# Performance work log

Measured on AMD Instinct MI355X. Metric: run time of the kernel, lower is better.

The kernel has to match this reference:

```python
import jax, jax.numpy as jnp
import numpy as np

N_NODES = 80000
N_EDGES = 1280000
IN_CH = 128
HID = 64
N_GRAPHS = 64
DROPOUT_P = 0.3


def setup_inputs() -> dict:
    key = jax.random.key(0)
    ks = jax.random.split(key, 12)
    x = jax.random.normal(ks[0], (N_NODES, IN_CH), dtype=jnp.float32)
    edge_index = jax.random.randint(ks[1], (2, N_EDGES), 0, N_NODES, dtype=jnp.int64 if jax.config.read('jax_enable_x64') else jnp.int32)
    batch = jnp.sort(jax.random.randint(ks[2], (N_NODES,), 0, N_GRAPHS))
    def lin(k, fan_in, fan_out):
        lim = 1.0 / np.sqrt(fan_in)
        kw, kb = jax.random.split(k)
        W = jax.random.uniform(kw, (fan_in, fan_out), minval=-lim, maxval=lim, dtype=jnp.float32)
        b = jax.random.uniform(kb, (fan_out,), minval=-lim, maxval=lim, dtype=jnp.float32)
        return W, b
    W1, b1 = lin(ks[3], IN_CH, HID)
    W2, b2 = lin(ks[4], HID, HID)
    W3, b3 = lin(ks[5], HID, HID)
    Wm1, bm1 = lin(ks[6], HID, HID)
    Wm2, bm2 = lin(ks[7], HID, 1)
    return {"x": x, "edge_index": edge_index, "batch": batch,
            "W1": W1, "b1": b1, "W2": W2, "b2": b2, "W3": W3, "b3": b3,
            "Wm1": Wm1, "bm1": bm1, "Wm2": Wm2, "bm2": bm2}


def _gcn_conv(x, W, b, src, dst, deg_inv_sqrt):
    # PyG GCNConv: h = X W; add self-loops; norm_e = d^-1/2[src] * d^-1/2[dst]
    h = x @ W  # [N, F]
    norm = deg_inv_sqrt[src] * deg_inv_sqrt[dst]  # [E]
    agg = jax.ops.segment_sum(h[src] * norm[:, None], dst, num_segments=x.shape[0])
    agg = agg + h * (deg_inv_sqrt * deg_inv_sqrt)[:, None]  # self-loop term d^-1
    return agg + b


def _dropout(x, key, p):
    keep = jax.random.bernoulli(key, 1.0 - p, x.shape)
    return jnp.where(keep, x / (1.0 - p), 0.0)


def reference(x, edge_index, batch, W1, b1, W2, b2, W3, b3, Wm1, bm1, Wm2, bm2):
    src, dst = edge_index[0], edge_index[1]
    N = x.shape[0]
    # in-degree on dst, +1 for self-loop (PyG default normalization)
    deg = jax.ops.segment_sum(jnp.ones_like(dst, dtype=x.dtype), dst, num_segments=N) + 1.0
    deg_inv_sqrt = jax.lax.rsqrt(deg)

    dk = jax.random.split(jax.random.key(42), 4)
    h = _dropout(jax.nn.relu(_gcn_conv(x, W1, b1, src, dst, deg_inv_sqrt)), dk[0], DROPOUT_P)
    h = _dropout(jax.nn.relu(_gcn_conv(h, W2, b2, src, dst, deg_inv_sqrt)), dk[1], DROPOUT_P)
    h = _dropout(jax.nn.relu(_gcn_conv(h, W3, b3, src, dst, deg_inv_sqrt)), dk[2], DROPOUT_P)

    # global mean pool per graph
    sums = jax.ops.segment_sum(h, batch, num_segments=N_GRAPHS)
    counts = jax.ops.segment_sum(jnp.ones((N,), dtype=h.dtype), batch, num_segments=N_GRAPHS)
    pooled = sums / jnp.maximum(counts, 1.0)[:, None]  # [G, HID]

    # MLP head: Linear -> ReLU -> Dropout -> Linear
    m = jax.nn.relu(pooled @ Wm1 + bm1)
    m = _dropout(m, dk[3], DROPOUT_P)
    return m @ Wm2 + bm2  # [G, 1]
```

## Files before the change

### kernel.cpp

```cpp
#include <hip/hip_runtime.h>
#include <hip/hip_fp8.h>
#include <stdint.h>

#define HID 64
#define INCH 128
#define NGRAPH 64
#define KEEPP 0.7f
#define SCAN_B 256

typedef __attribute__((ext_vector_type(8))) short short8;
typedef __attribute__((ext_vector_type(4))) float floatx4;
typedef unsigned short ushort_t;

__device__ __forceinline__ uint8_t f2e4(float f) {
  __hip_fp8_e4m3 t(f);
  return (uint8_t)t.__x;
}
__device__ __forceinline__ float e42f(uint8_t b) {
  __hip_fp8_e4m3 t;
  t.__x = (__hip_fp8_storage_t)b;
  return (float)t;
}

__host__ __device__ inline void tf2x32(uint32_t k0, uint32_t k1,
                                       uint32_t& x0, uint32_t& x1) {
  const uint32_t ks2 = k0 ^ k1 ^ 0x1BD11BDAu;
#define ROTL32(v, d) (((v) << (d)) | ((v) >> (32 - (d))))
#define TF_RND(r) { x0 += x1; x1 = ROTL32(x1, r); x1 ^= x0; }
  x0 += k0; x1 += k1;
  TF_RND(13) TF_RND(15) TF_RND(26) TF_RND(6)
  x0 += k1;  x1 += ks2 + 1u;
  TF_RND(17) TF_RND(29) TF_RND(16) TF_RND(24)
  x0 += ks2; x1 += k0 + 2u;
  TF_RND(13) TF_RND(15) TF_RND(26) TF_RND(6)
  x0 += k0;  x1 += k1 + 3u;
  TF_RND(17) TF_RND(29) TF_RND(16) TF_RND(24)
  x0 += k1;  x1 += ks2 + 4u;
  TF_RND(13) TF_RND(15) TF_RND(26) TF_RND(6)
  x0 += ks2; x1 += k0 + 5u;
#undef TF_RND
#undef ROTL32
}

__device__ __forceinline__ bool keep_mask(uint32_t k0, uint32_t k1, uint32_t idx) {
  uint32_t x0 = 0u, x1 = idx;
  tf2x32(k0, k1, x0, x1);
  uint32_t bits = x0 ^ x1;
  float u = __uint_as_float((bits >> 9) | 0x3f800000u) - 1.0f;
  return u < KEEPP;
}

__global__ void k_hist(const int* __restrict__ dst, int E, int* __restrict__ counts) {
  int e = blockIdx.x * blockDim.x + threadIdx.x;
  if (e < E) atomicAdd(&counts[dst[e]], 1);
}

__global__ __launch_bounds__(SCAN_B) void k_scan1d(const int* __restrict__ counts,
                                                   int* __restrict__ bsum,
                                                   float* __restrict__ dinv, int N) {
  int i = blockIdx.x * SCAN_B + threadIdx.x;
  int v = 0;
  if (i < N) {
    v = counts[i];
    dinv[i] = rsqrtf((float)v + 1.0f);
  }
  int r = v;
  for (int off = 32; off > 0; off >>= 1) r += __shfl_down(r, off);
  __shared__ int ws[4];
  if ((threadIdx.x & 63) == 0) ws[threadIdx.x >> 6] = r;
  __syncthreads();
  if (threadIdx.x == 0) bsum[blockIdx.x] = ws[0] + ws[1] + ws[2] + ws[3];
}

__device__ __forceinline__ void wsplit_one(const float* __restrict__ W,
                                           short8* __restrict__ Wh,
                                           short8* __restrict__ Wl, int i) {
  int lane = i & 63, f = i >> 6;
  int kc = f >> 2, ct = f & 3;
  int kbase = kc * 32 + ((lane >> 4) << 3);
  int n = ct * 16 + (lane & 15);
  short8 h, l;
#pragma unroll
  for (int j = 0; j < 8; ++j) {
    float w = W[(size_t)(kbase + j) * HID + n];
    uint32_t u = __float_as_uint(w);
    h[j] = (short)(u >> 16);
    float r = w - __uint_as_float(u & 0xFFFF0000u);
    l[j] = (short)(__float_as_uint(r) >> 16);
  }
  Wh[i] = h;
  Wl[i] = l;
}

__global__ __launch_bounds__(1024) void k_scan2w(const int* __restrict__ bsum,
                                                 int* __restrict__ bpre, int B,
                                                 const float* __restrict__ W1,
                                                 short8* __restrict__ Wh1, short8* __restrict__ Wl1,
                                                 const float* __restrict__ W2,
                                                 short8* __restrict__ Wh2, short8* __restrict__ Wl2,
                                                 const float* __restrict__ W3,
                                                 short8* __restrict__ Wh3, short8* __restrict__ Wl3) {
  if (blockIdx.x == 0) {
    __shared__ int s[1024];
    int tid = threadIdx.x;
    int v = (tid < B) ? bsum[tid] : 0;
    s[tid] = v;
    __syncthreads();
    for (int off = 1; off < 1024; off <<= 1) {
      int t = (tid >= off) ? s[tid - off] : 0;
      __syncthreads();
      s[tid] += t;
      __syncthreads();
    }
    if (tid < B) bpre[tid] = s[tid] - v;
    return;
  }
  int b = blockIdx.x - 1;
  int tid = threadIdx.x;
  if (b == 0) {
    wsplit_one(W1, Wh1, Wl1, tid);
  } else if (b == 1 && tid < 512) {
    wsplit_one(W2, Wh2, Wl2, tid);
  } else if (b == 2 && tid < 512) {
    wsplit_one(W3, Wh3, Wl3, tid);
  }
}

__global__ __launch_bounds__(SCAN_B) void k_scan3(const int* __restrict__ counts,
                                                  const int* __restrict__ bpre,
                                                  int* __restrict__ row_off,
                                                  int* __restrict__ cursor,
                                                  int N, int E) {
  __shared__ int s[SCAN_B];
  int tid = threadIdx.x;
  int i = blockIdx.x * SCAN_B + tid;
  int v = (i < N) ? counts[i] : 0;
  s[tid] = v;
  __syncthreads();
  for (int off = 1; off < SCAN_B; off <<= 1) {
    int t = (tid >= off) ? s[tid - off] : 0;
    __syncthreads();
    s[tid] += t;
    __syncthreads();
  }
  if (i < N) {
    int excl = bpre[blockIdx.x] + s[tid] - v;
    row_off[i] = excl;
    cursor[i] = excl;
  }
  if (i == 0) row_off[N] = E;
}

template <int K>
__device__ __forceinline__ void mgemm_tile(const float* __restrict__ A,
                                           const short8* __restrict__ Wh,
                                           const short8* __restrict__ Wl,
                                           uint8_t* __restrict__ C, int N,
                                           int tile) {
  constexpr int KC = K / 32;
  const int lane = threadIdx.x & 63;
  const int wv = threadIdx.x >> 6;
  const int m = lane & 15;
  const int q = lane >> 4;
  const int row0 = tile * 64 + wv * 16;
  if (row0 >= N) return;
  const int arow = min(row0 + m, N - 1);
  const float* __restrict__ ap = A + (size_t)arow * K + (q << 3);

  floatx4 acc[4];
#pragma unroll
  for (int ct = 0; ct < 4; ++ct) acc[ct] = (floatx4){0.f, 0.f, 0.f, 0.f};

#pragma unroll
  for (int kc = 0; kc < KC; ++kc) {
    const floatx4* apv = (const floatx4*)(ap + kc * 32);
    floatx4 x0 = apv[0];
    floatx4 x1 = apv[1];
    short8 ah, al;
#pragma unroll
    for (int j = 0; j < 4; ++j) {
      uint32_t u = __float_as_uint(x0[j]);
      ah[j] = (short)(u >> 16);
      float r = x0[j] - __uint_as_float(u & 0xFFFF0000u);
      al[j] = (short)(__float_as_uint(r) >> 16);
    }
#pragma unroll
    for (int j = 0; j < 4; ++j) {
      uint32_t u = __float_as_uint(x1[j]);
      ah[4 + j] = (short)(u >> 16);
      float r = x1[j] - __uint_as_float(u & 0xFFFF0000u);
      al[4 + j] = (short)(__float_as_uint(r) >> 16);
    }
#pragma unroll
    for (int ct = 0; ct < 4; ++ct) {
      short8 bh = Wh[(kc * 4 + ct) * 64 + lane];
      short8 bl = Wl[(kc * 4 + ct) * 64 + lane];
      acc[ct] = __builtin_amdgcn_mfma_f32_16x16x32_bf16(ah, bh, acc[ct], 0, 0, 0);
      acc[ct] = __builtin_amdgcn_mfma_f32_16x16x32_bf16(ah, bl, acc[ct], 0, 0, 0);
      acc[ct] = __builtin_amdgcn_mfma_f32_16x16x32_bf16(al, bh, acc[ct], 0, 0, 0);
    }
  }

  uint8_t* __restrict__ cp = C + (size_t)row0 * HID;
#pragma unroll
  for (int ct = 0; ct < 4; ++ct)
#pragma unroll
    for (int r = 0; r < 4; ++r) {
      int rr = (q << 2) + r;
      if (row0 + rr < N) cp[(size_t)rr * HID + ct * 16 + m] = f2e4(acc[ct][r]);
    }
}

template <int K>
__global__ __launch_bounds__(256) void k_mgemm_build(
    const float* __restrict__ A, const short8* __restrict__ Wh,
    const short8* __restrict__ Wl, uint8_t* __restrict__ C, int N,
    const int* __restrict__ src, const int* __restrict__ dst,
    const float* __restrict__ dinv, int* __restrict__ cursor,
    int2* __restrict__ csr, int E, int build_blocks, int gemm_blocks) {
  const long T = (long)build_blocks + gemm_blocks;
  const long b = (long)blockIdx.x;
  const long gb = (b * gemm_blocks) / T;
  const bool is_g = (((b + 1) * gemm_blocks) / T) != gb;
  if (!is_g) {
    int bb = (int)(b - gb);
    int e = bb * 256 + (int)threadIdx.x;
    if (e < E) {
      int s = src[e], d = dst[e];
      int pos = atomicAdd(&cursor[d], 1);
      csr[pos] = make_int2(s, __float_as_int(dinv[s] * dinv[d]));
    }
    return;
  }
  mgemm_tile<K>(A, Wh, Wl, C, N, (int)gb);
}

template <int K>
__global__ __launch_bounds__(256) void k_mgemm(const float* __restrict__ A,
                                               const short8* __restrict__ Wh,
                                               const short8* __restrict__ Wl,
                                               uint8_t* __restrict__ C, int N) {
  mgemm_tile<K>(A, Wh, Wl, C, N, (int)blockIdx.x);
}

__global__ __launch_bounds__(256) void k_gather(const uint8_t* __restrict__ tmp,
                                                const int* __restrict__ row_off,
                                                const int2* __restrict__ csr,
                                                const float* __restrict__ dinv,
                                                const float* __restrict__ bias,
                                                float* __restrict__ outh, int N,
                                                uint32_t k0, uint32_t k1) {
  const int node = blockIdx.x * 4 + (threadIdx.x >> 6);
  const int lane = threadIdx.x & 63;
  if (node >= N) return;
  const int beg = __builtin_amdgcn_readfirstlane(row_off[node]);
  const int end = __builtin_amdgcn_readfirstlane(row_off[node + 1]);
  float acc0 = 0.0f, acc1 = 0.0f, acc2 = 0.0f, acc3 = 0.0f;
  int j = beg;
  for (; j + 7 < end; j += 8) {
    int2 p0 = csr[j],     p1 = csr[j + 1], p2 = csr[j + 2], p3 = csr[j + 3];
    int2 p4 = csr[j + 4], p5 = csr[j + 5], p6 = csr[j + 6], p7 = csr[j + 7];
    float v0 = e42f(tmp[(size_t)p0.x * HID + lane]);
    float v1 = e42f(tmp[(size_t)p1.x * HID + lane]);
    float v2 = e42f(tmp[(size_t)p2.x * HID + lane]);
    float v3 = e42f(tmp[(size_t)p3.x * HID + lane]);
    float v4 = e42f(tmp[(size_t)p4.x * HID + lane]);
    float v5 = e42f(tmp[(size_t)p5.x * HID + lane]);
    float v6 = e42f(tmp[(size_t)p6.x * HID + lane]);
    float v7 = e42f(tmp[(size_t)p7.x * HID + lane]);
    acc0 = fmaf(v0, __int_as_float(p0.y), acc0);
    acc1 = fmaf(v1, __int_as_float(p1.y), acc1);
    acc2 = fmaf(v2, __int_as_float(p2.y), acc2);
    acc3 = fmaf(v3, __int_as_float(p3.y), acc3);
    acc0 = fmaf(v4, __int_as_float(p4.y), acc0);
    acc1 = fmaf(v5, __int_as_float(p5.y), acc1);
    acc2 = fmaf(v6, __int_as_float(p6.y), acc2);
    acc3 = fmaf(v7, __int_as_float(p7.y), acc3);
  }
  for (; j + 1 < end; j += 2) {
    int2 p0 = csr[j], p1 = csr[j + 1];
    float v0 = e42f(tmp[(size_t)p0.x * HID + lane]);
    float v1 = e42f(tmp[(size_t)p1.x * HID + lane]);
    acc0 = fmaf(v0, __int_as_float(p0.y), acc0);
    acc1 = fmaf(v1, __int_as_float(p1.y), acc1);
  }
  if (j < end) {
    int2 p0 = csr[j];
    acc2 = fmaf(e42f(tmp[(size_t)p0.x * HID + lane]), __int_as_float(p0.y), acc2);
  }
  float acc = (acc0 + acc1) + (acc2 + acc3);
  const float dnode = dinv[node];
  const int idx = node * HID + lane;
  float v = acc + e42f(tmp[idx]) * dnode * dnode + bias[lane];
  v = fmaxf(v, 0.0f);
  v = keep_mask(k0, k1, (uint32_t)idx) ? v / KEEPP : 0.0f;
  outh[idx] = v;
}

__global__ __launch_bounds__(256) void k_pool(const float* __restrict__ h,
                                              const int* __restrict__ batch,
                                              float* __restrict__ sums,
                                              float* __restrict__ cnts, int N) {
  __shared__ float ls[NGRAPH * HID];
  __shared__ float lc[NGRAPH];
  for (int i = threadIdx.x; i < NGRAPH * HID; i += 256) ls[i] = 0.0f;
  if (threadIdx.x < NGRAPH) lc[threadIdx.x] = 0.0f;
  __syncthreads();
  const int lane = threadIdx.x & 63;
  const int wave = threadIdx.x >> 6;
  int per = (N + gridDim.x - 1) / gridDim.x;
  int beg = blockIdx.x * per;
  int end = min(N, beg + per);
  for (int i = beg + wave; i < end; i += 4) {
    int g = batch[i];
    atomicAdd(&ls[g * HID + lane], h[(size_t)i * HID + lane]);
    if (lane == 0) atomicAdd(&lc[g], 1.0f);
  }
  __syncthreads();
  for (int i = threadIdx.x; i < NGRAPH * HID; i += 256)
    if (ls[i] != 0.0f) atomicAdd(&sums[i], ls[i]);
  if (threadIdx.x < NGRAPH && lc[threadIdx.x] != 0.0f)
    atomicAdd(&cnts[threadIdx.x], lc[threadIdx.x]);
}

__global__ __launch_bounds__(256) void k_head(const float* __restrict__ sums,
                                              const float* __restrict__ cnts,
                                              const float* __restrict__ Wm1,
                                              const float* __restrict__ bm1,
                                              const float* __restrict__ Wm2,
                                              const float* __restrict__ bm2,
                                              float* __restrict__ out,
                                              uint32_t k0, uint32_t k1) {
  __shared__ float pooled[NGRAPH * HID];
  __shared__ float m[NGRAPH * HID];
  for (int i = threadIdx.x; i < NGRAPH * HID; i += 256) {
    int g = i >> 6;
    pooled[i] = sums[i] / fmaxf(cnts[g], 1.0f);
  }
  __syncthreads();
  for (int i = threadIdx.x; i < NGRAPH * HID; i += 256) {
    int g = i >> 6, j = i & 63;
    float acc = bm1[j];
#pragma unroll 8
    for (int k = 0; k < HID; ++k)
      acc = fmaf(pooled[g * HID + k], Wm1[k * HID + j], acc);
    acc = fmaxf(acc, 0.0f);
    m[i] = keep_mask(k0, k1, (uint32_t)i) ? acc / KEEPP : 0.0f;
  }
  __syncthreads();
  if (threadIdx.x < NGRAPH) {
    int g = threadIdx.x;
    float acc = bm2[0];
#pragma unroll 8
    for (int j = 0; j < HID; ++j)
      acc = fmaf(m[g * HID + j], Wm2[j], acc);
    out[g] = acc;
  }
}

extern "C" void kernel_launch(void* const* d_in, const int* in_sizes, int n_in,
                              void* d_out, int out_size, void* d_ws, size_t ws_size,
                              hipStream_t stream) {
  const float* x     = (const float*)d_in[0];
  const int*   ei    = (const int*)d_in[1];
  const int*   batch = (const int*)d_in[2];
  const float* W1 = (const float*)d_in[3];
  const float* b1 = (const float*)d_in[4];
  const float* W2 = (const float*)d_in[5];
  const float* b2 = (const float*)d_in[6];
  const float* W3 = (const float*)d_in[7];
  const float* b3 = (const float*)d_in[8];
  const float* Wm1 = (const float*)d_in[9];
  const float* bm1 = (const float*)d_in[10];
  const float* Wm2 = (const float*)d_in[11];
  const float* bm2 = (const float*)d_in[12];
  float* out = (float*)d_out;

  const int N = in_sizes[0] / INCH;
  const int E = in_sizes[1] / 2;
  const int* src = ei;
  const int* dst = ei + E;
  const int NB = (N + SCAN_B - 1) / SCAN_B;

  char* ws = (char*)d_ws;
  size_t off = 0;
  uint8_t* B0 = (uint8_t*)(ws + off); off += (size_t)N * HID;
  off = (off + 15) & ~(size_t)15;
  float* B1      = (float*)(ws + off); off += (size_t)N * HID * 4;
  float* dinv    = (float*)(ws + off); off += (size_t)N * 4;
  int*   counts  = (int*)  (ws + off); off += (size_t)N * 4;
  int*   row_off = (int*)  (ws + off); off += ((size_t)N + 4) * 4;
  int*   cursor  = (int*)  (ws + off); off += (size_t)N * 4;
  int*   bsum    = (int*)  (ws + off); off += 1024 * 4;
  int*   bpre    = (int*)  (ws + off); off += 1024 * 4;
  int2*  csr     = (int2*) (ws + off); off += (size_t)E * 8;
  float* sums    = (float*)(ws + off); off += NGRAPH * HID * 4;
  float* cnts    = (float*)(ws + off); off += NGRAPH * 4;
  off = (off + 15) & ~(size_t)15;
  short8* Wh1 = (short8*)(ws + off); off += 1024 * 16;
  short8* Wl1 = (short8*)(ws + off); off += 1024 * 16;
  short8* Wh2 = (short8*)(ws + off); off += 512 * 16;
  short8* Wl2 = (short8*)(ws + off); off += 512 * 16;
  short8* Wh3 = (short8*)(ws + off); off += 512 * 16;
  short8* Wl3 = (short8*)(ws + off); off += 512 * 16;

  uint32_t dk[4][2];
  for (uint32_t i = 0; i < 4; ++i) {
    uint32_t a = 0u, b = i;
    tf2x32(0u, 42u, a, b);
    dk[i][0] = a; dk[i][1] = b;
  }

  hipMemsetAsync(counts, 0, (size_t)N * sizeof(int), stream);
  k_hist<<<(E + 255) / 256, 256, 0, stream>>>(dst, E, counts);
  k_scan1d<<<NB, SCAN_B, 0, stream>>>(counts, bsum, dinv, N);
  k_scan2w<<<4, 1024, 0, stream>>>(bsum, bpre, NB,
                                   W1, Wh1, Wl1, W2, Wh2, Wl2, W3, Wh3, Wl3);
  k_scan3<<<NB, SCAN_B, 0, stream>>>(counts, bpre, row_off, cursor, N, E);

  const int build_grid = (E + 255) / 256;
  const int mg_grid    = (N + 63) / 64;
  const int gath_grid  = (N + 3) / 4;

  k_mgemm_build<INCH><<<build_grid + mg_grid, 256, 0, stream>>>(
      x, Wh1, Wl1, B0, N, src, dst, dinv, cursor, csr, E, build_grid, mg_grid);
  k_gather<<<gath_grid, 256, 0, stream>>>(B0, row_off, csr, dinv, b1,
                                          B1, N, dk[0][0], dk[0][1]);
  k_mgemm<HID><<<mg_grid, 256, 0, stream>>>(B1, Wh2, Wl2, B0, N);
  k_gather<<<gath_grid, 256, 0, stream>>>(B0, row_off, csr, dinv, b2,
                                          B1, N, dk[1][0], dk[1][1]);
  k_mgemm<HID><<<mg_grid, 256, 0, stream>>>(B1, Wh3, Wl3, B0, N);
  k_gather<<<gath_grid, 256, 0, stream>>>(B0, row_off, csr, dinv, b3,
                                          B1, N, dk[2][0], dk[2][1]);

  hipMemsetAsync(sums, 0, (NGRAPH * HID + NGRAPH) * sizeof(float), stream);
  k_pool<<<256, 256, 0, stream>>>(B1, batch, sums, cnts, N);
  k_head<<<1, 256, 0, stream>>>(sums, cnts, Wm1, bm1, Wm2, bm2, out,
                                dk[3][0], dk[3][1]);
  (void)n_in; (void)out_size; (void)ws_size;
}
```

Before: 410.3 us.

## Gather four edges per wave with 4-byte fp8 loads and shuffle reduction

Changes the gather kernel so each wavefront splits into four 16-lane groups. Each group handles a different edge and loads 4 fp8 channels with a single 32-bit load, instead of every lane loading one byte of the same edge row. Partial sums are combined across groups with xor shuffles, and each lane then writes its channel in a permuted order. This is meant to cut the number of memory instructions and raise memory-level parallelism on the byte-granular random gathers, at the cost of the shuffle reduction and predicated tail handling.

```diff
diff --git a/kernel.cpp b/kernel.cpp
--- a/kernel.cpp
+++ b/kernel.cpp
@@ -252,46 +252,40 @@
                                                 uint32_t k0, uint32_t k1) {
   const int node = blockIdx.x * 4 + (threadIdx.x >> 6);
   const int lane = threadIdx.x & 63;
+  const int q = lane >> 4;
+  const int sl = lane & 15;
   if (node >= N) return;
   const int beg = __builtin_amdgcn_readfirstlane(row_off[node]);
   const int end = __builtin_amdgcn_readfirstlane(row_off[node + 1]);
-  float acc0 = 0.0f, acc1 = 0.0f, acc2 = 0.0f, acc3 = 0.0f;
-  int j = beg;
-  for (; j + 7 < end; j += 8) {
-    int2 p0 = csr[j],     p1 = csr[j + 1], p2 = csr[j + 2], p3 = csr[j + 3];
-    int2 p4 = csr[j + 4], p5 = csr[j + 5], p6 = csr[j + 6], p7 = csr[j + 7];
-    float v0 = e42f(tmp[(size_t)p0.x * HID + lane]);
-    float v1 = e42f(tmp[(size_t)p1.x * HID + lane]);
-    float v2 = e42f(tmp[(size_t)p2.x * HID + lane]);
-    float v3 = e42f(tmp[(size_t)p3.x * HID + lane]);
-    float v4 = e42f(tmp[(size_t)p4.x * HID + lane]);
-    float v5 = e42f(tmp[(size_t)p5.x * HID + lane]);
-    float v6 = e42f(tmp[(size_t)p6.x * HID + lane]);
-    float v7 = e42f(tmp[(size_t)p7.x * HID + lane]);
-    acc0 = fmaf(v0, __int_as_float(p0.y), acc0);
-    acc1 = fmaf(v1, __int_as_float(p1.y), acc1);
-    acc2 = fmaf(v2, __int_as_float(p2.y), acc2);
-    acc3 = fmaf(v3, __int_as_float(p3.y), acc3);
-    acc0 = fmaf(v4, __int_as_float(p4.y), acc0);
-    acc1 = fmaf(v5, __int_as_float(p5.y), acc1);
-    acc2 = fmaf(v6, __int_as_float(p6.y), acc2);
-    acc3 = fmaf(v7, __int_as_float(p7.y), acc3);
-  }
-  for (; j + 1 < end; j += 2) {
-    int2 p0 = csr[j], p1 = csr[j + 1];
-    float v0 = e42f(tmp[(size_t)p0.x * HID + lane]);
-    float v1 = e42f(tmp[(size_t)p1.x * HID + lane]);
-    acc0 = fmaf(v0, __int_as_float(p0.y), acc0);
-    acc1 = fmaf(v1, __int_as_float(p1.y), acc1);
-  }
-  if (j < end) {
-    int2 p0 = csr[j];
-    acc2 = fmaf(e42f(tmp[(size_t)p0.x * HID + lane]), __int_as_float(p0.y), acc2);
-  }
-  float acc = (acc0 + acc1) + (acc2 + acc3);
+
+  float a0 = 0.f, a1 = 0.f, a2 = 0.f, a3 = 0.f;
+  for (int j = beg; j < end; j += 8) {
+    int e0 = j + q, e1 = j + 4 + q;
+    bool v0 = e0 < end, v1 = e1 < end;
+    int2 p0 = csr[v0 ? e0 : beg];
+    int2 p1 = csr[v1 ? e1 : beg];
+    float w0 = v0 ? __int_as_float(p0.y) : 0.0f;
+    float w1 = v1 ? __int_as_float(p1.y) : 0.0f;
+    uint32_t r0 = *(const uint32_t*)(tmp + (size_t)p0.x * HID + sl * 4);
+    uint32_t r1 = *(const uint32_t*)(tmp + (size_t)p1.x * HID + sl * 4);
+    a0 = fmaf(e42f((uint8_t)(r0      )), w0, a0);
+    a1 = fmaf(e42f((uint8_t)(r0 >>  8)), w0, a1);
+    a2 = fmaf(e42f((uint8_t)(r0 >> 16)), w0, a2);
+    a3 = fmaf(e42f((uint8_t)(r0 >> 24)), w0, a3);
+    a0 = fmaf(e42f((uint8_t)(r1      )), w1, a0);
+    a1 = fmaf(e42f((uint8_t)(r1 >>  8)), w1, a1);
+    a2 = fmaf(e42f((uint8_t)(r1 >> 16)), w1, a2);
+    a3 = fmaf(e42f((uint8_t)(r1 >> 24)), w1, a3);
+  }
+  a0 += __shfl_xor(a0, 16); a0 += __shfl_xor(a0, 32);
+  a1 += __shfl_xor(a1, 16); a1 += __shfl_xor(a1, 32);
+  a2 += __shfl_xor(a2, 16); a2 += __shfl_xor(a2, 32);
+  a3 += __shfl_xor(a3, 16); a3 += __shfl_xor(a3, 32);
+  float acc = (q == 0) ? a0 : (q == 1) ? a1 : (q == 2) ? a2 : a3;
+  const int ch = sl * 4 + q;
   const float dnode = dinv[node];
-  const int idx = node * HID + lane;
-  float v = acc + e42f(tmp[idx]) * dnode * dnode + bias[lane];
+  const int idx = node * HID + ch;
+  float v = acc + e42f(tmp[(size_t)node * HID + ch]) * dnode * dnode + bias[ch];
   v = fmaxf(v, 0.0f);
   v = keep_mask(k0, k1, (uint32_t)idx) ? v / KEEPP : 0.0f;
   outh[idx] = v;
```

New measurement: 418.4 us. About the same (+2.0%).
